# Kernel tuning notes

Hardware: AMD Instinct MI355X
Metric: run time of the kernel (lower is better)

Reference implementation:

```python
import jax, jax.numpy as jnp
import numpy as np

N, E, G, C, H = 40000, 640000, 40, 128, 2
D = H * C  # flattened per-node width after each GAT layer
SLOPE = 0.2
EPS = 1e-5

def _leaky(x):
    return jnp.where(x >= 0, x, SLOPE * x)

def _gat(x, W, al, ar, res, src, dst):
    # DGL GATConv (bias=False, residual=True): fc -> per-head attn logits -> edge softmax -> weighted scatter-sum
    h = (x @ W).reshape(N, H, C)
    el = (h * al[None]).sum(-1)                      # (N, H)
    er = (h * ar[None]).sum(-1)                      # (N, H)
    e = _leaky(el[src] + er[dst])                    # (E, H) attention logits
    m = jax.ops.segment_max(e, dst, num_segments=N)  # stable edge softmax per dst node
    ex = jnp.exp(e - m[dst])
    s = jax.ops.segment_sum(ex, dst, num_segments=N)
    a = ex / (s[dst] + 1e-9)                         # (E, H)
    out = jax.ops.segment_sum(h[src] * a[:, :, None], dst, num_segments=N)  # (N, H, C)
    return (out + res).reshape(N, D)

def _united_norm(x, gids, cnt, lbn, lgn, lnn, gamma, beta):
    # learnable per-feature combination of batch-, graph- and node-norm (UnitedNormCommon)
    bn = (x - x.mean(0)) * jax.lax.rsqrt(x.var(0) + EPS)
    gm = jax.ops.segment_sum(x, gids, num_segments=G) / cnt[:, None]
    d = x - gm[gids]
    gv = jax.ops.segment_sum(d * d, gids, num_segments=G) / cnt[:, None]
    gn = d * jax.lax.rsqrt(gv[gids] + EPS)
    nnrm = (x - x.mean(-1, keepdims=True)) * jax.lax.rsqrt(x.var(-1, keepdims=True) + EPS)
    return gamma * (lbn * bn + lgn * gn + lnn * nnrm) + beta

def _forward(node_feats, src, dst, graph_ids, W0, W1, W2, al0, al1, al2,
             ar0, ar1, ar2, resW0, g0, g1, g2, b0, b1, b2,
             lbn0, lbn1, lbn2, lgn0, lgn1, lgn2, lnn0, lnn1, lnn2):
    cnt = jax.ops.segment_sum(jnp.ones((N,), node_feats.dtype), graph_ids, num_segments=G)
    Ws = (W0, W1, W2); als = (al0, al1, al2); ars = (ar0, ar1, ar2)
    gs = (g0, g1, g2); bs = (b0, b1, b2)
    lbns = (lbn0, lbn1, lbn2); lgns = (lgn0, lgn1, lgn2); lnns = (lnn0, lnn1, lnn2)
    x = node_feats
    emb = None
    for i in range(3):  # fixed small layer count
        res = (x @ resW0).reshape(N, H, C) if i == 0 else x.reshape(N, H, C)
        x = _gat(x, Ws[i], als[i], ars[i], res, src, dst)
        x = _leaky(_united_norm(x, graph_ids, cnt, lbns[i], lgns[i], lnns[i], gs[i], bs[i]))
        head_mean = x.reshape(N, H, C).mean(1)  # (N, C) mean over heads
        emb = jax.ops.segment_sum(head_mean, graph_ids, num_segments=G) / cnt[:, None]  # mean_nodes readout
    return _leaky(emb)  # jumping_mode=None -> LeakyReLU of last embedding, (G, C)

def setup_inputs():
    ks = jax.random.split(jax.random.key(0), 16)
    s = 0.05
    inp = {
        "node_feats": jax.random.normal(ks[0], (N, C), jnp.float32),
        "src": jax.random.randint(ks[1], (E,), 0, N, dtype=jnp.int32),
        "dst": jax.random.randint(ks[2], (E,), 0, N, dtype=jnp.int32),
        "graph_ids": jnp.arange(N, dtype=jnp.int32) // (N // G),
        "W0": jax.random.normal(ks[3], (C, D), jnp.float32) * s,
        "W1": jax.random.normal(ks[4], (D, D), jnp.float32) * s,
        "W2": jax.random.normal(ks[5], (D, D), jnp.float32) * s,
        "resW0": jax.random.normal(ks[6], (C, D), jnp.float32) * s,
    }
    for i in range(3):
        inp[f"al{i}"] = jax.random.normal(ks[7 + i], (H, C), jnp.float32) * s
        inp[f"ar{i}"] = jax.random.normal(ks[10 + i], (H, C), jnp.float32) * s
        inp[f"g{i}"] = jnp.ones((D,), jnp.float32)
        inp[f"b{i}"] = jnp.zeros((D,), jnp.float32)
        inp[f"lbn{i}"] = jnp.full((D,), 1.0 / 3.0, jnp.float32)
        inp[f"lgn{i}"] = jnp.full((D,), 1.0 / 3.0, jnp.float32)
        inp[f"lnn{i}"] = jnp.full((D,), 1.0 / 3.0, jnp.float32)
    return inp

def reference(node_feats, src, dst, graph_ids, W0, W1, W2, resW0,
              al0, al1, al2, ar0, ar1, ar2, g0, g1, g2, b0, b1, b2,
              lbn0, lbn1, lbn2, lgn0, lgn1, lgn2, lnn0, lnn1, lnn2):
    return _forward(node_feats, src, dst, graph_ids, W0, W1, W2, al0, al1, al2,
                    ar0, ar1, ar2, resW0, g0, g1, g2, b0, b1, b2,
                    lbn0, lbn1, lbn2, lgn0, lgn1, lgn2, lnn0, lnn1, lnn2)
```

## Files before the change

kernel.cpp:

```cpp
#include <hip/hip_runtime.h>
#include <math.h>

#define NN 40000
#define NPAD 40064
#define NE 640000
#define NG 40
#define NC 128
#define ND 256
#define SLOPEF 0.2f
#define EPSF 1e-5f
#define SCAN_NB 157

typedef short bf16x8 __attribute__((ext_vector_type(8)));
typedef float f32x4 __attribute__((ext_vector_type(4)));

static __device__ __forceinline__ float lrelu(float x){ return x >= 0.0f ? x : SLOPEF * x; }

static __device__ __forceinline__ unsigned int bfpair(float a, float b){
  unsigned int ua = __float_as_uint(a);
  ua = (ua + 0x7fffu + ((ua >> 16) & 1u)) >> 16;
  unsigned int ub = __float_as_uint(b);
  ub = (ub + 0x7fffu + ((ub >> 16) & 1u)) >> 16;
  return ua | (ub << 16);
}
static __device__ __forceinline__ unsigned short bf1(float x){
  unsigned int u = __float_as_uint(x);
  return (unsigned short)((u + 0x7fffu + ((u >> 16) & 1u)) >> 16);
}
static __device__ __forceinline__ float4 cvt4(ushort4 v){
  float4 o;
  o.x = __uint_as_float(((unsigned)v.x) << 16);
  o.y = __uint_as_float(((unsigned)v.y) << 16);
  o.z = __uint_as_float(((unsigned)v.z) << 16);
  o.w = __uint_as_float(((unsigned)v.w) << 16);
  return o;
}

static __device__ __forceinline__ void gload16(const void* gsrc, void* lds){
  __builtin_amdgcn_global_load_lds(
      (const __attribute__((address_space(1))) void*)gsrc,
      (__attribute__((address_space(3))) void*)lds, 16, 0, 0);
}

__global__ __launch_bounds__(256) void k_zero(int* __restrict__ deg, int* __restrict__ cur,
                                              int* __restrict__ cnt, int* __restrict__ gmn,
                                              int* __restrict__ gmx, float* __restrict__ gsum,
                                              float* __restrict__ gsq, float* __restrict__ obuf){
  int i = blockIdx.x*256 + threadIdx.x;
  int stride = gridDim.x*256;
  for(int j = i; j < NN; j += stride){ deg[j] = 0; cur[j] = 0; }
  for(int j = i; j < NG; j += stride){ cnt[j] = 0; gmn[j] = 0x7f7f7f7f; gmx[j] = -1; }
  for(int j = i; j < NG*ND; j += stride){ gsum[j] = 0.0f; gsq[j] = 0.0f; }
  for(int j = i; j < NG*NC; j += stride){ obuf[j] = 0.0f; }
}

__global__ void k_deg_hist(const int* __restrict__ dst, int* __restrict__ deg){
  int e = blockIdx.x*256 + threadIdx.x;
  if(e < NE) atomicAdd(&deg[dst[e]], 1);
}

__global__ __launch_bounds__(256) void k_graph_stats(const int* __restrict__ gid, int* __restrict__ cnt,
                                                     int* __restrict__ gmn, int* __restrict__ gmx){
  __shared__ int lc[NG], lmn[NG], lmx[NG];
  int tid = threadIdx.x;
  for(int i = tid; i < NG; i += 256){ lc[i] = 0; lmn[i] = 0x7f7f7f7f; lmx[i] = -1; }
  __syncthreads();
  int n = blockIdx.x*256 + tid;
  if(n < NN){
    int g = gid[n];
    atomicAdd(&lc[g], 1);
    atomicMin(&lmn[g], n);
    atomicMax(&lmx[g], n);
  }
  __syncthreads();
  for(int i = tid; i < NG; i += 256){
    if(lc[i] > 0){
      atomicAdd(&cnt[i], lc[i]);
      atomicMin(&gmn[i], lmn[i]);
      atomicMax(&gmx[i], lmx[i]);
    }
  }
}

__global__ __launch_bounds__(256) void k_scan_a(const int* __restrict__ deg, int* __restrict__ bsum){
  int tid = threadIdx.x;
  int i = blockIdx.x*256 + tid;
  int v = (i < NN) ? deg[i] : 0;
#pragma unroll
  for(int off = 32; off >= 1; off >>= 1) v += __shfl_xor(v, off);
  __shared__ int ws[4];
  if((tid & 63) == 0) ws[tid >> 6] = v;
  __syncthreads();
  if(tid == 0) bsum[blockIdx.x] = ws[0] + ws[1] + ws[2] + ws[3];
}

__global__ __launch_bounds__(256) void k_scan_b(int* __restrict__ bsum, int* __restrict__ boff,
                                                int* __restrict__ rowstart){
  __shared__ int lds[256];
  int tid = threadIdx.x;
  int v = (tid < SCAN_NB) ? bsum[tid] : 0;
  lds[tid] = v;
  __syncthreads();
  for(int off = 1; off < 256; off <<= 1){
    int t = (tid >= off) ? lds[tid - off] : 0;
    __syncthreads();
    lds[tid] += t;
    __syncthreads();
  }
  if(tid < SCAN_NB) boff[tid] = lds[tid] - v;
  if(tid == SCAN_NB - 1) rowstart[NN] = lds[tid];
}

__global__ __launch_bounds__(256) void k_scan_c(const int* __restrict__ deg, const int* __restrict__ boff,
                                                int* __restrict__ rowstart){
  __shared__ int lds[256];
  int tid = threadIdx.x;
  int i = blockIdx.x*256 + tid;
  int v = (i < NN) ? deg[i] : 0;
  lds[tid] = v;
  __syncthreads();
  for(int off = 1; off < 256; off <<= 1){
    int t = (tid >= off) ? lds[tid - off] : 0;
    __syncthreads();
    lds[tid] += t;
    __syncthreads();
  }
  if(i < NN) rowstart[i] = boff[blockIdx.x] + lds[tid] - v;
}

__global__ void k_fill(const int* __restrict__ src, const int* __restrict__ dst,
                       const int* __restrict__ rowstart, int* __restrict__ cur, int* __restrict__ srcS){
  int e = blockIdx.x*256 + threadIdx.x;
  if(e < NE){
    int d = dst[e];
    int slot = rowstart[d] + atomicAdd(&cur[d], 1);
    srcS[slot] = src[e];
  }
}

template<int K>
__global__ __launch_bounds__(256) void k_cvt_a(const float* __restrict__ in, unsigned int* __restrict__ out){
  int i = blockIdx.x*256 + threadIdx.x;
  long e8 = (long)i * 8;
  if(e8 >= (long)NPAD * K) return;
  int row = (int)(e8 / K);
  int col = (int)(e8 - (long)row * K);
  uint4 o;
  if(row < NN){
    const float4* p = (const float4*)(in + (size_t)row*K + col);
    float4 v0 = p[0], v1 = p[1];
    o.x = bfpair(v0.x, v0.y); o.y = bfpair(v0.z, v0.w);
    o.z = bfpair(v1.x, v1.y); o.w = bfpair(v1.z, v1.w);
  } else {
    o = make_uint4(0,0,0,0);
  }
  ((uint4*)out)[i] = o;
}

template<int K>
__global__ __launch_bounds__(256) void k_cvt_wt(const float* __restrict__ W, unsigned short* __restrict__ Wt){
  int i = blockIdx.x*256 + threadIdx.x;
  int c  = i / (K/8);
  int k0 = (i - c*(K/8)) * 8;
  float v[8];
#pragma unroll
  for(int u = 0; u < 8; ++u) v[u] = W[(size_t)(k0+u)*ND + c];
  uint4 o;
  o.x = bfpair(v[0], v[1]); o.y = bfpair(v[2], v[3]);
  o.z = bfpair(v[4], v[5]); o.w = bfpair(v[6], v[7]);
  *((uint4*)(Wt + (size_t)c*K + k0)) = o;
}

__global__ __launch_bounds__(256) void k_cvt_wt0(const float* __restrict__ W0, const float* __restrict__ Wr,
                                                 unsigned short* __restrict__ Wt){
  int i = blockIdx.x*256 + threadIdx.x;
  int c  = i / (NC/8);
  int k0 = (i - c*(NC/8)) * 8;
  const float* W = (c < ND) ? W0 : Wr;
  int cc = c & (ND-1);
  float v[8];
#pragma unroll
  for(int u = 0; u < 8; ++u) v[u] = W[(size_t)(k0+u)*ND + cc];
  uint4 o;
  o.x = bfpair(v[0], v[1]); o.y = bfpair(v[2], v[3]);
  o.z = bfpair(v[4], v[5]); o.w = bfpair(v[6], v[7]);
  *((uint4*)(Wt + (size_t)c*NC + k0)) = o;
}

template<int K, int MODE>
__global__ __launch_bounds__(256) void k_gemm_bf16(const unsigned short* __restrict__ A,
                                                   const unsigned short* __restrict__ Bt,
                                                   float* __restrict__ Cf,
                                                   unsigned short* __restrict__ Cb){
  __shared__ unsigned short As[128*32];
  __shared__ unsigned short Bs[128*32];
  int t = threadIdx.x;
  int lane = t & 63, wid = t >> 6;
  int wm = wid & 1, wn = wid >> 1;
  int r = lane & 15, g = lane >> 4;
  int bm = blockIdx.x * 128;
  int bn = blockIdx.y * 128;
  int srow = t >> 2, scol = (t & 3) * 8;

  int aoff[4], boff[4];
#pragma unroll
  for(int m = 0; m < 4; ++m) aoff[m] = ((wm*64 + m*16 + r) << 5) + (g << 3);
#pragma unroll
  for(int n = 0; n < 4; ++n) boff[n] = ((wn*64 + n*16 + r) << 5) + (g << 3);

  f32x4 acc[4][4] = {};

  for(int k0 = 0; k0 < K; k0 += 32){
    gload16(A + (size_t)(bm + srow)*K      + k0 + scol, (char*)As + t*16);
    gload16(A + (size_t)(bm + 64 + srow)*K + k0 + scol, (char*)As + 4096 + t*16);
    gload16(Bt + (size_t)(bn + srow)*K      + k0 + scol, (char*)Bs + t*16);
    gload16(Bt + (size_t)(bn + 64 + srow)*K + k0 + scol, (char*)Bs + 4096 + t*16);
    __syncthreads();

    bf16x8 af[4], bfv[4];
#pragma unroll
    for(int m = 0; m < 4; ++m) af[m] = *(const bf16x8*)&As[aoff[m]];
#pragma unroll
    for(int n = 0; n < 4; ++n) bfv[n] = *(const bf16x8*)&Bs[boff[n]];
#pragma unroll
    for(int m = 0; m < 4; ++m)
#pragma unroll
      for(int n = 0; n < 4; ++n)
        acc[m][n] = __builtin_amdgcn_mfma_f32_16x16x32_bf16(af[m], bfv[n], acc[m][n], 0, 0, 0);
    __syncthreads();
  }

#pragma unroll
  for(int m = 0; m < 4; ++m){
    int row0 = bm + wm*64 + m*16 + g*4;
#pragma unroll
    for(int n = 0; n < 4; ++n){
      int col = bn + wn*64 + n*16 + r;
#pragma unroll
      for(int i = 0; i < 4; ++i){
        if(row0 + i < NN){
          if(MODE == 1){
            Cb[(size_t)(row0+i)*ND + col] = bf1(acc[m][n][i]);
          } else {
            if(col < ND) Cb[(size_t)(row0+i)*ND + col] = bf1(acc[m][n][i]);
            else         Cf[(size_t)(row0+i)*ND + (col - ND)] = acc[m][n][i];
          }
        }
      }
    }
  }
}

__global__ __launch_bounds__(256) void k_elr(const unsigned short* __restrict__ Hm, const float* __restrict__ al,
                                             const float* __restrict__ ar, float* __restrict__ el,
                                             float* __restrict__ er){
  int n = blockIdx.x*4 + (threadIdx.x >> 6);
  int lane = threadIdx.x & 63;
  if(n >= NN) return;
  float4 hv = cvt4(((const ushort4*)(Hm + (size_t)n*ND))[lane]);
  float4 a  = ((const float4*)al)[lane];
  float4 b  = ((const float4*)ar)[lane];
  float sl = hv.x*a.x + hv.y*a.y + hv.z*a.z + hv.w*a.w;
  float sr = hv.x*b.x + hv.y*b.y + hv.z*b.z + hv.w*b.w;
#pragma unroll
  for(int off = 16; off >= 1; off >>= 1){ sl += __shfl_xor(sl, off); sr += __shfl_xor(sr, off); }
  if(lane == 0){ el[n*2+0] = sl; er[n*2+0] = sr; }
  if(lane == 32){ el[n*2+1] = sl; er[n*2+1] = sr; }
}

__global__ __launch_bounds__(256) void k_attn(const unsigned short* __restrict__ Hm, const float* __restrict__ el,
                                              const float* __restrict__ er, const int* __restrict__ rowstart,
                                              const int* __restrict__ srcS, const float* __restrict__ res,
                                              float* __restrict__ out){
  int n = blockIdx.x*4 + (threadIdx.x >> 6);
  int lane = threadIdx.x & 63;
  if(n >= NN) return;
  int rs = rowstart[n], re = rowstart[n+1];
  int deg = re - rs;
  float4 acc = ((const float4*)(res + (size_t)n*ND))[lane];
  if(deg > 0){
    float er0 = er[n*2], er1 = er[n*2+1];
    if(deg <= 64){
      int s = srcS[rs + (lane < deg ? lane : 0)];
      float e0 = -1e30f, e1 = -1e30f;
      if(lane < deg){
        e0 = lrelu(el[s*2]   + er0);
        e1 = lrelu(el[s*2+1] + er1);
      }
      float m0 = e0, m1 = e1;
#pragma unroll
      for(int off = 32; off >= 1; off >>= 1){ m0 = fmaxf(m0, __shfl_xor(m0, off)); m1 = fmaxf(m1, __shfl_xor(m1, off)); }
      float x0 = (lane < deg) ? expf(e0 - m0) : 0.0f;
      float x1 = (lane < deg) ? expf(e1 - m1) : 0.0f;
      float s0 = x0, s1 = x1;
#pragma unroll
      for(int off = 32; off >= 1; off >>= 1){ s0 += __shfl_xor(s0, off); s1 += __shfl_xor(s1, off); }
      x0 *= 1.0f/(s0 + 1e-9f);
      x1 *= 1.0f/(s1 + 1e-9f);
      bool h1 = (lane >= 32);
      for(int j0 = 0; j0 < deg; j0 += 4){
        int sj0 = __shfl(s, j0+0), sj1 = __shfl(s, j0+1);
        int sj2 = __shfl(s, j0+2), sj3 = __shfl(s, j0+3);
        ushort4 g0 = ((const ushort4*)(Hm + (size_t)sj0*ND))[lane];
        ushort4 g1 = ((const ushort4*)(Hm + (size_t)sj1*ND))[lane];
        ushort4 g2 = ((const ushort4*)(Hm + (size_t)sj2*ND))[lane];
        ushort4 g3 = ((const ushort4*)(Hm + (size_t)sj3*ND))[lane];
        float a00 = __shfl(x0, j0+0), a10 = __shfl(x1, j0+0);
        float a01 = __shfl(x0, j0+1), a11 = __shfl(x1, j0+1);
        float a02 = __shfl(x0, j0+2), a12 = __shfl(x1, j0+2);
        float a03 = __shfl(x0, j0+3), a13 = __shfl(x1, j0+3);
        float w0 = h1 ? a10 : a00;
        float w1 = h1 ? a11 : a01;
        float w2 = h1 ? a12 : a02;
        float w3 = h1 ? a13 : a03;
        float4 v0 = cvt4(g0), v1 = cvt4(g1), v2 = cvt4(g2), v3 = cvt4(g3);
        acc.x += w0*v0.x + w1*v1.x + w2*v2.x + w3*v3.x;
        acc.y += w0*v0.y + w1*v1.y + w2*v2.y + w3*v3.y;
        acc.z += w0*v0.z + w1*v1.z + w2*v2.z + w3*v3.z;
        acc.w += w0*v0.w + w1*v1.w + w2*v2.w + w3*v3.w;
      }
    } else {
      float m0 = -1e30f, m1 = -1e30f;
      for(int j = lane; j < deg; j += 64){
        int s = srcS[rs + j];
        m0 = fmaxf(m0, lrelu(el[s*2]   + er0));
        m1 = fmaxf(m1, lrelu(el[s*2+1] + er1));
      }
#pragma unroll
      for(int off = 32; off >= 1; off >>= 1){ m0 = fmaxf(m0, __shfl_xor(m0, off)); m1 = fmaxf(m1, __shfl_xor(m1, off)); }
      float s0 = 0.0f, s1 = 0.0f;
      for(int j = lane; j < deg; j += 64){
        int s = srcS[rs + j];
        s0 += expf(lrelu(el[s*2]   + er0) - m0);
        s1 += expf(lrelu(el[s*2+1] + er1) - m1);
      }
#pragma unroll
      for(int off = 32; off >= 1; off >>= 1){ s0 += __shfl_xor(s0, off); s1 += __shfl_xor(s1, off); }
      float inv = (lane < 32) ? 1.0f/(s0 + 1e-9f) : 1.0f/(s1 + 1e-9f);
      float mh  = (lane < 32) ? m0 : m1;
      for(int j = 0; j < deg; ++j){
        int s = srcS[rs + j];
        float e = (lane < 32) ? lrelu(el[s*2] + er0) : lrelu(el[s*2+1] + er1);
        float a = expf(e - mh) * inv;
        float4 hv = cvt4(((const ushort4*)(Hm + (size_t)s*ND))[lane]);
        acc.x += a*hv.x; acc.y += a*hv.y; acc.z += a*hv.z; acc.w += a*hv.w;
      }
    }
  }
  ((float4*)(out + (size_t)n*ND))[lane] = acc;
}

__global__ __launch_bounds__(256) void k_gstats(const float* __restrict__ X, const int* __restrict__ gid,
                                                float* __restrict__ gsum, float* __restrict__ gsq){
  __shared__ f32x4 reds[256];
  __shared__ f32x4 redq[256];
  int tid = threadIdx.x;
  int f4 = tid & 63;
  int r  = tid >> 6;
  int n0 = blockIdx.x * 125;
  int g0 = gid[n0];
  f32x4 s0 = {0,0,0,0}, q0 = {0,0,0,0};
  f32x4 s1 = {0,0,0,0}, q1 = {0,0,0,0};
  int cg1 = -1;
  for(int n = n0 + r; n < n0 + 125; n += 4){
    int g = gid[n];
    f32x4 v = *(const f32x4*)(X + (size_t)n*ND + f4*4);
    if(g == g0){ s0 += v; q0 += v*v; }
    else {
      if(g != cg1){
        if(cg1 >= 0){
#pragma unroll
          for(int j = 0; j < 4; ++j){
            atomicAdd(&gsum[cg1*ND + f4*4 + j], s1[j]);
            atomicAdd(&gsq [cg1*ND + f4*4 + j], q1[j]);
          }
        }
        cg1 = g; s1 = (f32x4){0,0,0,0}; q1 = (f32x4){0,0,0,0};
      }
      s1 += v; q1 += v*v;
    }
  }
  if(cg1 >= 0){
#pragma unroll
    for(int j = 0; j < 4; ++j){
      atomicAdd(&gsum[cg1*ND + f4*4 + j], s1[j]);
      atomicAdd(&gsq [cg1*ND + f4*4 + j], q1[j]);
    }
  }
  reds[tid] = s0; redq[tid] = q0;
  __syncthreads();
  if(r == 0){
    f32x4 ts = reds[f4] + reds[f4+64] + reds[f4+128] + reds[f4+192];
    f32x4 tq = redq[f4] + redq[f4+64] + redq[f4+128] + redq[f4+192];
#pragma unroll
    for(int j = 0; j < 4; ++j){
      atomicAdd(&gsum[g0*ND + f4*4 + j], ts[j]);
      atomicAdd(&gsq [g0*ND + f4*4 + j], tq[j]);
    }
  }
}

__global__ void k_finstats(float* __restrict__ gsum, float* __restrict__ gsq,
                           const int* __restrict__ cnt, float* __restrict__ gmean, float* __restrict__ grs,
                           float* __restrict__ bnm, float* __restrict__ bnrs){
  int d = threadIdx.x;
  float ts = 0.0f, tq = 0.0f;
  for(int g = 0; g < NG; ++g){
    float c = (float)cnt[g];
    float s = gsum[g*ND + d], q = gsq[g*ND + d];
    gsum[g*ND + d] = 0.0f; gsq[g*ND + d] = 0.0f;
    ts += s; tq += q;
    float m = s / c;
    float v = q / c - m*m;
    gmean[g*ND + d] = m;
    grs[g*ND + d] = rsqrtf(fmaxf(v, 0.0f) + EPSF);
  }
  float bm = ts / (float)NN;
  float bv = tq / (float)NN - bm*bm;
  bnm[d] = bm;
  bnrs[d] = rsqrtf(fmaxf(bv, 0.0f) + EPSF);
}

template<int LAYER>
__global__ __launch_bounds__(256) void k_norm(const float* __restrict__ X, const int* __restrict__ gid,
    const float* __restrict__ gmean, const float* __restrict__ grs, const float* __restrict__ bnm,
    const float* __restrict__ bnrs, const float* __restrict__ gamma, const float* __restrict__ beta,
    const float* __restrict__ lbn, const float* __restrict__ lgn, const float* __restrict__ lnn,
    float* __restrict__ out, unsigned short* __restrict__ abf){
  int n = blockIdx.x*4 + (threadIdx.x >> 6);
  int lane = threadIdx.x & 63;
  if(n >= NPAD) return;
  if(n >= NN){
    if(LAYER < 2){ uint2 z = {0,0}; ((uint2*)(abf + (size_t)n*ND))[lane] = z; }
    return;
  }
  float4 v = ((const float4*)(X + (size_t)n*ND))[lane];
  float s = v.x + v.y + v.z + v.w;
  float q = v.x*v.x + v.y*v.y + v.z*v.z + v.w*v.w;
#pragma unroll
  for(int off = 32; off >= 1; off >>= 1){ s += __shfl_xor(s, off); q += __shfl_xor(q, off); }
  float nm = s * (1.0f/ND);
  float nv = q * (1.0f/ND) - nm*nm;
  float nrs = rsqrtf(fmaxf(nv, 0.0f) + EPSF);
  int g = gid[n];
  float4 gm = ((const float4*)(gmean + g*ND))[lane];
  float4 gr = ((const float4*)(grs   + g*ND))[lane];
  float4 bm = ((const float4*)bnm)[lane];
  float4 br = ((const float4*)bnrs)[lane];
  float4 ga = ((const float4*)gamma)[lane];
  float4 be = ((const float4*)beta)[lane];
  float4 lb = ((const float4*)lbn)[lane];
  float4 lg = ((const float4*)lgn)[lane];
  float4 ln = ((const float4*)lnn)[lane];
  float4 o;
  o.x = lrelu(ga.x*(lb.x*((v.x-bm.x)*br.x) + lg.x*((v.x-gm.x)*gr.x) + ln.x*((v.x-nm)*nrs)) + be.x);
  o.y = lrelu(ga.y*(lb.y*((v.y-bm.y)*br.y) + lg.y*((v.y-gm.y)*gr.y) + ln.y*((v.y-nm)*nrs)) + be.y);
  o.z = lrelu(ga.z*(lb.z*((v.z-bm.z)*br.z) + lg.z*((v.z-gm.z)*gr.z) + ln.z*((v.z-nm)*nrs)) + be.z);
  o.w = lrelu(ga.w*(lb.w*((v.w-bm.w)*br.w) + lg.w*((v.w-gm.w)*gr.w) + ln.w*((v.w-nm)*nrs)) + be.w);
  if(LAYER < 2){
    ((float4*)(out + (size_t)n*ND))[lane] = o;
    uint2 pk; pk.x = bfpair(o.x, o.y); pk.y = bfpair(o.z, o.w);
    ((uint2*)(abf + (size_t)n*ND))[lane] = pk;
  } else {
    float4 p;
    p.x = __shfl_xor(o.x, 32); p.y = __shfl_xor(o.y, 32);
    p.z = __shfl_xor(o.z, 32); p.w = __shfl_xor(o.w, 32);
    if(lane < 32){
      float4 hm;
      hm.x = 0.5f*(o.x + p.x); hm.y = 0.5f*(o.y + p.y);
      hm.z = 0.5f*(o.z + p.z); hm.w = 0.5f*(o.w + p.w);
      ((float4*)(out + (size_t)n*NC))[lane] = hm;
    }
  }
}

__global__ void k_readout_part(const float* __restrict__ HM, const int* __restrict__ gid,
                               const int* __restrict__ gmn, const int* __restrict__ gmx,
                               float* __restrict__ obuf){
  int g = blockIdx.x >> 3, part = blockIdx.x & 7;
  int c = threadIdx.x;
  int n0 = gmn[g], n1 = gmx[g] + 1;
  int len = n1 - n0;
  int beg = n0 + (int)(((long)len * part) >> 3);
  int end = n0 + (int)(((long)len * (part+1)) >> 3);
  float acc = 0.0f;
  for(int n = beg; n < end; ++n){
    if(gid[n] == g) acc += HM[(size_t)n*NC + c];
  }
  atomicAdd(&obuf[g*NC + c], acc);
}

__global__ void k_readout_fin(const float* __restrict__ obuf, const int* __restrict__ cnt,
                              float* __restrict__ outp){
  int i = blockIdx.x*128 + threadIdx.x;
  int g = i / NC;
  outp[i] = lrelu(obuf[i] / (float)cnt[g]);
}

extern "C" void kernel_launch(void* const* d_in, const int* in_sizes, int n_in,
                              void* d_out, int out_size, void* d_ws, size_t ws_size,
                              hipStream_t stream){
  const float* X0  = (const float*)d_in[0];
  const int* src   = (const int*)d_in[1];
  const int* dst   = (const int*)d_in[2];
  const int* gid   = (const int*)d_in[3];
  const float* Wm[3] = { (const float*)d_in[4], (const float*)d_in[5], (const float*)d_in[6] };
  const float* resW  = (const float*)d_in[7];
  const float *AL[3], *AR[3], *GA[3], *BE[3], *LB[3], *LG[3], *LN[3];
  for(int i = 0; i < 3; ++i){
    int b = 8 + i*7;
    AL[i] = (const float*)d_in[b];   AR[i] = (const float*)d_in[b+1];
    GA[i] = (const float*)d_in[b+2]; BE[i] = (const float*)d_in[b+3];
    LB[i] = (const float*)d_in[b+4]; LG[i] = (const float*)d_in[b+5]; LN[i] = (const float*)d_in[b+6];
  }
  float* out = (float*)d_out;

  float* wf = (float*)d_ws;
  float* Hb   = wf;                 wf += (size_t)NN*ND;
  float* XA   = wf;                 wf += (size_t)NN*ND;
  float* XB   = wf;                 wf += (size_t)NN*ND;
  float* RES  = wf;                 wf += (size_t)NN*ND;
  float* el   = wf;                 wf += (size_t)NN*2;
  float* er   = wf;                 wf += (size_t)NN*2;
  float* gsum = wf;                 wf += NG*ND;
  float* gsq  = wf;                 wf += NG*ND;
  float* gmean= wf;                 wf += NG*ND;
  float* grs  = wf;                 wf += NG*ND;
  float* bnm  = wf;                 wf += ND;
  float* bnrs = wf;                 wf += ND;
  float* obuf = wf;                 wf += NG*NC;
  unsigned short* Btw = (unsigned short*)wf; wf += (ND*ND)/2;
  int* ip = (int*)wf;
  int* deg      = ip;               ip += NN;
  int* rowstart = ip;               ip += NN + 1;
  int* cur      = ip;               ip += NN;
  int* srcS     = ip;               ip += NE;
  int* cnt      = ip;               ip += NG;
  int* gmn      = ip;               ip += NG;
  int* gmx      = ip;               ip += NG;
  int* bsum     = ip;               ip += SCAN_NB;
  int* boff     = ip;               ip += SCAN_NB;

  unsigned short* Hbf   = (unsigned short*)Hb;
  unsigned short* A0bf  = (unsigned short*)XA;
  unsigned short* ANbf  = (unsigned short*)RES;

  k_zero<<<SCAN_NB, 256, 0, stream>>>(deg, cur, cnt, gmn, gmx, gsum, gsq, obuf);
  k_deg_hist<<<(NE+255)/256, 256, 0, stream>>>(dst, deg);
  k_graph_stats<<<(NN+255)/256, 256, 0, stream>>>(gid, cnt, gmn, gmx);
  k_scan_a<<<SCAN_NB, 256, 0, stream>>>(deg, bsum);
  k_scan_b<<<1, 256, 0, stream>>>(bsum, boff, rowstart);
  k_scan_c<<<SCAN_NB, 256, 0, stream>>>(deg, boff, rowstart);
  k_fill<<<(NE+255)/256, 256, 0, stream>>>(src, dst, rowstart, cur, srcS);

  for(int L = 0; L < 3; ++L){
    if(L == 0){
      k_cvt_a<NC><<<(NPAD*NC/8 + 255)/256, 256, 0, stream>>>(X0, (unsigned int*)A0bf);
      k_cvt_wt0<<<(2*ND*NC/8)/256, 256, 0, stream>>>(Wm[0], resW, Btw);
      dim3 g0(NPAD/128, 4);
      k_gemm_bf16<NC,2><<<g0, 256, 0, stream>>>(A0bf, Btw, RES, Hbf);
    } else {
      k_cvt_wt<ND><<<(ND*ND/8)/256, 256, 0, stream>>>(Wm[L], Btw);
      dim3 g1(NPAD/128, 2);
      k_gemm_bf16<ND,1><<<g1, 256, 0, stream>>>(ANbf, Btw, nullptr, Hbf);
    }
    const float* resp = (L == 0) ? RES : XB;
    k_elr<<<NN/4, 256, 0, stream>>>(Hbf, AL[L], AR[L], el, er);
    k_attn<<<NN/4, 256, 0, stream>>>(Hbf, el, er, rowstart, srcS, resp, XA);
    k_gstats<<<NN/125, 256, 0, stream>>>(XA, gid, gsum, gsq);
    k_finstats<<<1, 256, 0, stream>>>(gsum, gsq, cnt, gmean, grs, bnm, bnrs);
    if(L == 0)      k_norm<0><<<NPAD/4, 256, 0, stream>>>(XA, gid, gmean, grs, bnm, bnrs, GA[0], BE[0], LB[0], LG[0], LN[0], XB, ANbf);
    else if(L == 1) k_norm<1><<<NPAD/4, 256, 0, stream>>>(XA, gid, gmean, grs, bnm, bnrs, GA[1], BE[1], LB[1], LG[1], LN[1], XB, ANbf);
    else            k_norm<2><<<NN/4, 256, 0, stream>>>(XA, gid, gmean, grs, bnm, bnrs, GA[2], BE[2], LB[2], LG[2], LN[2], RES, nullptr);
  }
  k_readout_part<<<NG*8, NC, 0, stream>>>(RES, gid, gmn, gmx, obuf);
  k_readout_fin<<<NG, NC, 0, stream>>>(obuf, cnt, out);
}
```

Measured before the change: 496.0 us.

## Fuse attention logit computation into GEMM epilogue and unroll neighbor gather

```diff
diff --git a/kernel.cpp b/kernel.cpp
--- a/kernel.cpp
+++ b/kernel.cpp
@@ -158,8 +158,10 @@
 }
 
 template<int K>
-__global__ __launch_bounds__(256) void k_cvt_wt(const float* __restrict__ W, unsigned short* __restrict__ Wt){
+__global__ __launch_bounds__(256) void k_cvt_wt(const float* __restrict__ W, unsigned short* __restrict__ Wt,
+                                                float4* __restrict__ elz){
   int i = blockIdx.x*256 + threadIdx.x;
+  for(int j = i; j < NPAD; j += gridDim.x*256) elz[j] = make_float4(0,0,0,0);
   int c  = i / (K/8);
   int k0 = (i - c*(K/8)) * 8;
   float v[8];
@@ -172,8 +174,9 @@
 }
 
 __global__ __launch_bounds__(256) void k_cvt_wt0(const float* __restrict__ W0, const float* __restrict__ Wr,
-                                                 unsigned short* __restrict__ Wt){
+                                                 unsigned short* __restrict__ Wt, float4* __restrict__ elz){
   int i = blockIdx.x*256 + threadIdx.x;
+  for(int j = i; j < NPAD; j += gridDim.x*256) elz[j] = make_float4(0,0,0,0);
   int c  = i / (NC/8);
   int k0 = (i - c*(NC/8)) * 8;
   const float* W = (c < ND) ? W0 : Wr;
@@ -191,7 +194,11 @@
 __global__ __launch_bounds__(256) void k_gemm_bf16(const unsigned short* __restrict__ A,
                                                    const unsigned short* __restrict__ Bt,
                                                    float* __restrict__ Cf,
-                                                   unsigned short* __restrict__ Cb){
+                                                   unsigned short* __restrict__ Cb,
+                                                   const float* __restrict__ al,
+                                                   const float* __restrict__ ar,
+                                                   float* __restrict__ el,
+                                                   float* __restrict__ er){
   __shared__ unsigned short As[128*32];
   __shared__ unsigned short Bs[128*32];
   int t = threadIdx.x;
@@ -249,23 +256,34 @@
       }
     }
   }
-}
-
-__global__ __launch_bounds__(256) void k_elr(const unsigned short* __restrict__ Hm, const float* __restrict__ al,
-                                             const float* __restrict__ ar, float* __restrict__ el,
-                                             float* __restrict__ er){
-  int n = blockIdx.x*4 + (threadIdx.x >> 6);
-  int lane = threadIdx.x & 63;
-  if(n >= NN) return;
-  float4 hv = cvt4(((const ushort4*)(Hm + (size_t)n*ND))[lane]);
-  float4 a  = ((const float4*)al)[lane];
-  float4 b  = ((const float4*)ar)[lane];
-  float sl = hv.x*a.x + hv.y*a.y + hv.z*a.z + hv.w*a.w;
-  float sr = hv.x*b.x + hv.y*b.y + hv.z*b.z + hv.w*b.w;
-#pragma unroll
-  for(int off = 16; off >= 1; off >>= 1){ sl += __shfl_xor(sl, off); sr += __shfl_xor(sr, off); }
-  if(lane == 0){ el[n*2+0] = sl; er[n*2+0] = sr; }
-  if(lane == 32){ el[n*2+1] = sl; er[n*2+1] = sr; }
+
+  if(MODE == 1 || bn < ND){
+    int head = (bn + wn*64) >= NC ? 1 : 0;
+    float alv[4], arv[4];
+#pragma unroll
+    for(int n = 0; n < 4; ++n){
+      int col = bn + wn*64 + n*16 + r;
+      alv[n] = al[col]; arv[n] = ar[col];
+    }
+#pragma unroll
+    for(int m = 0; m < 4; ++m){
+      int row0 = bm + wm*64 + m*16 + g*4;
+#pragma unroll
+      for(int i = 0; i < 4; ++i){
+        float pel = acc[m][0][i]*alv[0] + acc[m][1][i]*alv[1] + acc[m][2][i]*alv[2] + acc[m][3][i]*alv[3];
+        float per = acc[m][0][i]*arv[0] + acc[m][1][i]*arv[1] + acc[m][2][i]*arv[2] + acc[m][3][i]*arv[3];
+#pragma unroll
+        for(int off = 1; off < 16; off <<= 1){
+          pel += __shfl_xor(pel, off);
+          per += __shfl_xor(per, off);
+        }
+        if(r == 0 && row0 + i < NN){
+          atomicAdd(&el[(size_t)(row0+i)*2 + head], pel);
+          atomicAdd(&er[(size_t)(row0+i)*2 + head], per);
+        }
+      }
+    }
+  }
 }
 
 __global__ __launch_bounds__(256) void k_attn(const unsigned short* __restrict__ Hm, const float* __restrict__ el,
@@ -298,26 +316,22 @@
       x0 *= 1.0f/(s0 + 1e-9f);
       x1 *= 1.0f/(s1 + 1e-9f);
       bool h1 = (lane >= 32);
-      for(int j0 = 0; j0 < deg; j0 += 4){
-        int sj0 = __shfl(s, j0+0), sj1 = __shfl(s, j0+1);
-        int sj2 = __shfl(s, j0+2), sj3 = __shfl(s, j0+3);
-        ushort4 g0 = ((const ushort4*)(Hm + (size_t)sj0*ND))[lane];
-        ushort4 g1 = ((const ushort4*)(Hm + (size_t)sj1*ND))[lane];
-        ushort4 g2 = ((const ushort4*)(Hm + (size_t)sj2*ND))[lane];
-        ushort4 g3 = ((const ushort4*)(Hm + (size_t)sj3*ND))[lane];
-        float a00 = __shfl(x0, j0+0), a10 = __shfl(x1, j0+0);
-        float a01 = __shfl(x0, j0+1), a11 = __shfl(x1, j0+1);
-        float a02 = __shfl(x0, j0+2), a12 = __shfl(x1, j0+2);
-        float a03 = __shfl(x0, j0+3), a13 = __shfl(x1, j0+3);
-        float w0 = h1 ? a10 : a00;
-        float w1 = h1 ? a11 : a01;
-        float w2 = h1 ? a12 : a02;
-        float w3 = h1 ? a13 : a03;
-        float4 v0 = cvt4(g0), v1 = cvt4(g1), v2 = cvt4(g2), v3 = cvt4(g3);
-        acc.x += w0*v0.x + w1*v1.x + w2*v2.x + w3*v3.x;
-        acc.y += w0*v0.y + w1*v1.y + w2*v2.y + w3*v3.y;
-        acc.z += w0*v0.z + w1*v1.z + w2*v2.z + w3*v3.z;
-        acc.w += w0*v0.w + w1*v1.w + w2*v2.w + w3*v3.w;
+      for(int j0 = 0; j0 < deg; j0 += 8){
+        int sj[8];
+#pragma unroll
+        for(int u = 0; u < 8; ++u) sj[u] = __shfl(s, j0 + u);
+        ushort4 gv[8];
+#pragma unroll
+        for(int u = 0; u < 8; ++u) gv[u] = ((const ushort4*)(Hm + (size_t)sj[u]*ND))[lane];
+        float wa[8], wb[8];
+#pragma unroll
+        for(int u = 0; u < 8; ++u){ wa[u] = __shfl(x0, j0 + u); wb[u] = __shfl(x1, j0 + u); }
+#pragma unroll
+        for(int u = 0; u < 8; ++u){
+          float w = h1 ? wb[u] : wa[u];
+          float4 v = cvt4(gv[u]);
+          acc.x += w*v.x; acc.y += w*v.y; acc.z += w*v.z; acc.w += w*v.w;
+        }
       }
     } else {
       float m0 = -1e30f, m1 = -1e30f;
@@ -520,8 +534,8 @@
   float* XA   = wf;                 wf += (size_t)NN*ND;
   float* XB   = wf;                 wf += (size_t)NN*ND;
   float* RES  = wf;                 wf += (size_t)NN*ND;
-  float* el   = wf;                 wf += (size_t)NN*2;
-  float* er   = wf;                 wf += (size_t)NN*2;
+  float* el   = wf;                 wf += (size_t)NPAD*2;
+  float* er   = wf;                 wf += (size_t)NPAD*2;
   float* gsum = wf;                 wf += NG*ND;
   float* gsq  = wf;                 wf += NG*ND;
   float* gmean= wf;                 wf += NG*ND;
@@ -544,6 +558,7 @@
   unsigned short* Hbf   = (unsigned short*)Hb;
   unsigned short* A0bf  = (unsigned short*)XA;
   unsigned short* ANbf  = (unsigned short*)RES;
+  float4* elz = (float4*)el;
 
   k_zero<<<SCAN_NB, 256, 0, stream>>>(deg, cur, cnt, gmn, gmx, gsum, gsq, obuf);
   k_deg_hist<<<(NE+255)/256, 256, 0, stream>>>(dst, deg);
@@ -556,16 +571,15 @@
   for(int L = 0; L < 3; ++L){
     if(L == 0){
       k_cvt_a<NC><<<(NPAD*NC/8 + 255)/256, 256, 0, stream>>>(X0, (unsigned int*)A0bf);
-      k_cvt_wt0<<<(2*ND*NC/8)/256, 256, 0, stream>>>(Wm[0], resW, Btw);
+      k_cvt_wt0<<<(2*ND*NC/8)/256, 256, 0, stream>>>(Wm[0], resW, Btw, elz);
       dim3 g0(NPAD/128, 4);
-      k_gemm_bf16<NC,2><<<g0, 256, 0, stream>>>(A0bf, Btw, RES, Hbf);
+      k_gemm_bf16<NC,2><<<g0, 256, 0, stream>>>(A0bf, Btw, RES, Hbf, AL[0], AR[0], el, er);
     } else {
-      k_cvt_wt<ND><<<(ND*ND/8)/256, 256, 0, stream>>>(Wm[L], Btw);
+      k_cvt_wt<ND><<<(ND*ND/8)/256, 256, 0, stream>>>(Wm[L], Btw, elz);
       dim3 g1(NPAD/128, 2);
-      k_gemm_bf16<ND,1><<<g1, 256, 0, stream>>>(ANbf, Btw, nullptr, Hbf);
+      k_gemm_bf16<ND,1><<<g1, 256, 0, stream>>>(ANbf, Btw, nullptr, Hbf, AL[L], AR[L], el, er);
     }
     const float* resp = (L == 0) ? RES : XB;
-    k_elr<<<NN/4, 256, 0, stream>>>(Hbf, AL[L], AR[L], el, er);
     k_attn<<<NN/4, 256, 0, stream>>>(Hbf, el, er, rowstart, srcS, resp, XA);
     k_gstats<<<NN/125, 256, 0, stream>>>(XA, gid, gsum, gsq);
     k_finstats<<<1, 256, 0, stream>>>(gsum, gsq, cnt, gmean, grs, bnm, bnrs);
```

Measured after the change: 504.3 us. No clear change (+1.7%).

## Store intermediate activations and residuals in bf16 instead of fp32

Applied to the files above, without the earlier changes.

```diff
diff --git a/kernel.cpp b/kernel.cpp
--- a/kernel.cpp
+++ b/kernel.cpp
@@ -190,7 +190,7 @@
 template<int K, int MODE>
 __global__ __launch_bounds__(256) void k_gemm_bf16(const unsigned short* __restrict__ A,
                                                    const unsigned short* __restrict__ Bt,
-                                                   float* __restrict__ Cf,
+                                                   unsigned short* __restrict__ Cb2,
                                                    unsigned short* __restrict__ Cb){
   __shared__ unsigned short As[128*32];
   __shared__ unsigned short Bs[128*32];
@@ -243,7 +243,7 @@
             Cb[(size_t)(row0+i)*ND + col] = bf1(acc[m][n][i]);
           } else {
             if(col < ND) Cb[(size_t)(row0+i)*ND + col] = bf1(acc[m][n][i]);
-            else         Cf[(size_t)(row0+i)*ND + (col - ND)] = acc[m][n][i];
+            else         Cb2[(size_t)(row0+i)*ND + (col - ND)] = bf1(acc[m][n][i]);
           }
         }
       }
@@ -270,14 +270,14 @@
 
 __global__ __launch_bounds__(256) void k_attn(const unsigned short* __restrict__ Hm, const float* __restrict__ el,
                                               const float* __restrict__ er, const int* __restrict__ rowstart,
-                                              const int* __restrict__ srcS, const float* __restrict__ res,
-                                              float* __restrict__ out){
+                                              const int* __restrict__ srcS, const unsigned short* __restrict__ res,
+                                              unsigned short* __restrict__ out){
   int n = blockIdx.x*4 + (threadIdx.x >> 6);
   int lane = threadIdx.x & 63;
   if(n >= NN) return;
   int rs = rowstart[n], re = rowstart[n+1];
   int deg = re - rs;
-  float4 acc = ((const float4*)(res + (size_t)n*ND))[lane];
+  float4 acc = cvt4(((const ushort4*)(res + (size_t)n*ND))[lane]);
   if(deg > 0){
     float er0 = er[n*2], er1 = er[n*2+1];
     if(deg <= 64){
@@ -347,10 +347,11 @@
       }
     }
   }
-  ((float4*)(out + (size_t)n*ND))[lane] = acc;
-}
-
-__global__ __launch_bounds__(256) void k_gstats(const float* __restrict__ X, const int* __restrict__ gid,
+  uint2 pk; pk.x = bfpair(acc.x, acc.y); pk.y = bfpair(acc.z, acc.w);
+  ((uint2*)(out + (size_t)n*ND))[lane] = pk;
+}
+
+__global__ __launch_bounds__(256) void k_gstats(const unsigned short* __restrict__ X, const int* __restrict__ gid,
                                                 float* __restrict__ gsum, float* __restrict__ gsq){
   __shared__ f32x4 reds[256];
   __shared__ f32x4 redq[256];
@@ -364,7 +365,8 @@
   int cg1 = -1;
   for(int n = n0 + r; n < n0 + 125; n += 4){
     int g = gid[n];
-    f32x4 v = *(const f32x4*)(X + (size_t)n*ND + f4*4);
+    float4 vv = cvt4(*(const ushort4*)(X + (size_t)n*ND + f4*4));
+    f32x4 v = {vv.x, vv.y, vv.z, vv.w};
     if(g == g0){ s0 += v; q0 += v*v; }
     else {
       if(g != cg1){
@@ -422,19 +424,19 @@
 }
 
 template<int LAYER>
-__global__ __launch_bounds__(256) void k_norm(const float* __restrict__ X, const int* __restrict__ gid,
+__global__ __launch_bounds__(256) void k_norm(const unsigned short* __restrict__ X, const int* __restrict__ gid,
     const float* __restrict__ gmean, const float* __restrict__ grs, const float* __restrict__ bnm,
     const float* __restrict__ bnrs, const float* __restrict__ gamma, const float* __restrict__ beta,
     const float* __restrict__ lbn, const float* __restrict__ lgn, const float* __restrict__ lnn,
-    float* __restrict__ out, unsigned short* __restrict__ abf){
+    unsigned short* __restrict__ outb, float* __restrict__ outf){
   int n = blockIdx.x*4 + (threadIdx.x >> 6);
   int lane = threadIdx.x & 63;
   if(n >= NPAD) return;
   if(n >= NN){
-    if(LAYER < 2){ uint2 z = {0,0}; ((uint2*)(abf + (size_t)n*ND))[lane] = z; }
+    if(LAYER < 2){ uint2 z = {0,0}; ((uint2*)(outb + (size_t)n*ND))[lane] = z; }
     return;
   }
-  float4 v = ((const float4*)(X + (size_t)n*ND))[lane];
+  float4 v = cvt4(((const ushort4*)(X + (size_t)n*ND))[lane]);
   float s = v.x + v.y + v.z + v.w;
   float q = v.x*v.x + v.y*v.y + v.z*v.z + v.w*v.w;
 #pragma unroll
@@ -458,9 +460,8 @@
   o.z = lrelu(ga.z*(lb.z*((v.z-bm.z)*br.z) + lg.z*((v.z-gm.z)*gr.z) + ln.z*((v.z-nm)*nrs)) + be.z);
   o.w = lrelu(ga.w*(lb.w*((v.w-bm.w)*br.w) + lg.w*((v.w-gm.w)*gr.w) + ln.w*((v.w-nm)*nrs)) + be.w);
   if(LAYER < 2){
-    ((float4*)(out + (size_t)n*ND))[lane] = o;
     uint2 pk; pk.x = bfpair(o.x, o.y); pk.y = bfpair(o.z, o.w);
-    ((uint2*)(abf + (size_t)n*ND))[lane] = pk;
+    ((uint2*)(outb + (size_t)n*ND))[lane] = pk;
   } else {
     float4 p;
     p.x = __shfl_xor(o.x, 32); p.y = __shfl_xor(o.y, 32);
@@ -469,7 +470,7 @@
       float4 hm;
       hm.x = 0.5f*(o.x + p.x); hm.y = 0.5f*(o.y + p.y);
       hm.z = 0.5f*(o.z + p.z); hm.w = 0.5f*(o.w + p.w);
-      ((float4*)(out + (size_t)n*NC))[lane] = hm;
+      ((float4*)(outf + (size_t)n*NC))[lane] = hm;
     }
   }
 }
@@ -516,10 +517,10 @@
   float* out = (float*)d_out;
 
   float* wf = (float*)d_ws;
-  float* Hb   = wf;                 wf += (size_t)NN*ND;
-  float* XA   = wf;                 wf += (size_t)NN*ND;
-  float* XB   = wf;                 wf += (size_t)NN*ND;
-  float* RES  = wf;                 wf += (size_t)NN*ND;
+  unsigned short* Hbf  = (unsigned short*)wf;  wf += (size_t)NN*ND/2;
+  unsigned short* XAb  = (unsigned short*)wf;  wf += (size_t)NN*ND/2;
+  unsigned short* XBb  = (unsigned short*)wf;  wf += (size_t)NPAD*ND/2;
+  unsigned short* RESb = (unsigned short*)wf;  wf += (size_t)NN*ND/2;
   float* el   = wf;                 wf += (size_t)NN*2;
   float* er   = wf;                 wf += (size_t)NN*2;
   float* gsum = wf;                 wf += NG*ND;
@@ -541,9 +542,8 @@
   int* bsum     = ip;               ip += SCAN_NB;
   int* boff     = ip;               ip += SCAN_NB;
 
-  unsigned short* Hbf   = (unsigned short*)Hb;
-  unsigned short* A0bf  = (unsigned short*)XA;
-  unsigned short* ANbf  = (unsigned short*)RES;
+  unsigned short* A0bf = XAb;
+  float* HMf = (float*)RESb;
 
   k_zero<<<SCAN_NB, 256, 0, stream>>>(deg, cur, cnt, gmn, gmx, gsum, gsq, obuf);
   k_deg_hist<<<(NE+255)/256, 256, 0, stream>>>(dst, deg);
@@ -558,21 +558,21 @@
       k_cvt_a<NC><<<(NPAD*NC/8 + 255)/256, 256, 0, stream>>>(X0, (unsigned int*)A0bf);
       k_cvt_wt0<<<(2*ND*NC/8)/256, 256, 0, stream>>>(Wm[0], resW, Btw);
       dim3 g0(NPAD/128, 4);
-      k_gemm_bf16<NC,2><<<g0, 256, 0, stream>>>(A0bf, Btw, RES, Hbf);
+      k_gemm_bf16<NC,2><<<g0, 256, 0, stream>>>(A0bf, Btw, RESb, Hbf);
     } else {
       k_cvt_wt<ND><<<(ND*ND/8)/256, 256, 0, stream>>>(Wm[L], Btw);
       dim3 g1(NPAD/128, 2);
-      k_gemm_bf16<ND,1><<<g1, 256, 0, stream>>>(ANbf, Btw, nullptr, Hbf);
-    }
-    const float* resp = (L == 0) ? RES : XB;
+      k_gemm_bf16<ND,1><<<g1, 256, 0, stream>>>(XBb, Btw, nullptr, Hbf);
+    }
+    const unsigned short* resp = (L == 0) ? RESb : XBb;
     k_elr<<<NN/4, 256, 0, stream>>>(Hbf, AL[L], AR[L], el, er);
-    k_attn<<<NN/4, 256, 0, stream>>>(Hbf, el, er, rowstart, srcS, resp, XA);
-    k_gstats<<<NN/125, 256, 0, stream>>>(XA, gid, gsum, gsq);
+    k_attn<<<NN/4, 256, 0, stream>>>(Hbf, el, er, rowstart, srcS, resp, XAb);
+    k_gstats<<<NN/125, 256, 0, stream>>>(XAb, gid, gsum, gsq);
     k_finstats<<<1, 256, 0, stream>>>(gsum, gsq, cnt, gmean, grs, bnm, bnrs);
-    if(L == 0)      k_norm<0><<<NPAD/4, 256, 0, stream>>>(XA, gid, gmean, grs, bnm, bnrs, GA[0], BE[0], LB[0], LG[0], LN[0], XB, ANbf);
-    else if(L == 1) k_norm<1><<<NPAD/4, 256, 0, stream>>>(XA, gid, gmean, grs, bnm, bnrs, GA[1], BE[1], LB[1], LG[1], LN[1], XB, ANbf);
-    else            k_norm<2><<<NN/4, 256, 0, stream>>>(XA, gid, gmean, grs, bnm, bnrs, GA[2], BE[2], LB[2], LG[2], LN[2], RES, nullptr);
-  }
-  k_readout_part<<<NG*8, NC, 0, stream>>>(RES, gid, gmn, gmx, obuf);
+    if(L == 0)      k_norm<0><<<NPAD/4, 256, 0, stream>>>(XAb, gid, gmean, grs, bnm, bnrs, GA[0], BE[0], LB[0], LG[0], LN[0], XBb, nullptr);
+    else if(L == 1) k_norm<1><<<NPAD/4, 256, 0, stream>>>(XAb, gid, gmean, grs, bnm, bnrs, GA[1], BE[1], LB[1], LG[1], LN[1], XBb, nullptr);
+    else            k_norm<2><<<NN/4, 256, 0, stream>>>(XAb, gid, gmean, grs, bnm, bnrs, GA[2], BE[2], LB[2], LG[2], LN[2], nullptr, HMf);
+  }
+  k_readout_part<<<NG*8, NC, 0, stream>>>(HMf, gid, gmn, gmx, obuf);
   k_readout_fin<<<NG, NC, 0, stream>>>(obuf, cnt, out);
 }
```

Result: faster. 480.0 us (-3.2%).
